# Kernel tuning notes

Measured on AMD Instinct MI355X. Metric: run time of the kernel, lower is better.

The kernel has to match this reference:

```python
import jax, jax.numpy as jnp
import numpy as np

D = 1024
H = 16
EPS = 1e-5


def setup_inputs() -> dict:
    key = jax.random.key(0)
    ks = jax.random.split(key, 6)
    B, T, d = 4, 2048, D
    s = 0.02
    return {
        "x": jax.random.normal(ks[0], (B, T, d), jnp.float32),
        "w_attn": jax.random.normal(ks[1], (d, 3 * d), jnp.float32) * s,
        "w_o": jax.random.normal(ks[2], (d, d), jnp.float32) * s,
        "ln1_g": jnp.ones((d,), jnp.float32),
        "ln1_b": jnp.zeros((d,), jnp.float32),
        "ln2_g": jnp.ones((d,), jnp.float32),
        "ln2_b": jnp.zeros((d,), jnp.float32),
        "w_fc": jax.random.normal(ks[3], (d, 4 * d), jnp.float32) * s,
        "b_fc": jnp.zeros((4 * d,), jnp.float32),
        "w_proj": jax.random.normal(ks[4], (4 * d, d), jnp.float32) * s,
        "b_proj": jnp.zeros((d,), jnp.float32),
    }


def _layernorm(x, g, b):
    mu = jnp.mean(x, axis=-1, keepdims=True)
    var = jnp.mean(jnp.square(x - mu), axis=-1, keepdims=True)
    return (x - mu) * jax.lax.rsqrt(var + EPS) * g + b


def _attention(x, w_attn, w_o):
    B, T, d = x.shape
    hd = d // H
    qkv = x @ w_attn  # [B,T,3d]
    q, k, v = jnp.split(qkv, 3, axis=-1)
    q = q.reshape(B, T, H, hd).transpose(0, 2, 1, 3)  # [B,H,T,hd]
    k = k.reshape(B, T, H, hd).transpose(0, 2, 1, 3)
    v = v.reshape(B, T, H, hd).transpose(0, 2, 1, 3)
    att = jnp.einsum("bhqd,bhkd->bhqk", q, k) * (1.0 / np.sqrt(hd))
    mask = jnp.tril(jnp.ones((T, T), bool))
    att = jnp.where(mask, att, jnp.float32(-jnp.inf))
    att = jax.nn.softmax(att, axis=-1)
    y = jnp.einsum("bhqk,bhkd->bhqd", att, v)
    y = y.transpose(0, 2, 1, 3).reshape(B, T, d)
    return y @ w_o


def reference(x, w_attn, w_o, ln1_g, ln1_b, ln2_g, ln2_b, w_fc, b_fc, w_proj, b_proj):
    x = x + _attention(_layernorm(x, ln1_g, ln1_b), w_attn, w_o)
    h = _layernorm(x, ln2_g, ln2_b)
    h = jax.nn.gelu(h @ w_fc + b_fc, approximate=True)
    return x + h @ w_proj + b_proj
```

## Files before the change

kernel.cpp:

```cpp
#include <hip/hip_runtime.h>
#include <math.h>

#define D_MODEL 1024
#define NHEAD   16
#define HDIM    64
#define SEQ     2048
#define BATCH   4
#define NROWS   (BATCH*SEQ)

using bf16x8 = __attribute__((ext_vector_type(8))) short;
using bf16x4 = __attribute__((ext_vector_type(4))) short;
using f32x4  = __attribute__((ext_vector_type(4))) float;

__device__ __forceinline__ unsigned short f2bf(float f) {
    unsigned u = __float_as_uint(f);
    u += 0x7fffu + ((u >> 16) & 1u);
    return (unsigned short)(u >> 16);
}
__device__ __forceinline__ float bf2f(unsigned short h) {
    unsigned u = ((unsigned)h) << 16;
    return __uint_as_float(u);
}

#define ASYNC_COPY16(g, l) \
    __builtin_amdgcn_global_load_lds((__attribute__((address_space(1))) const void*)(g), \
                                     (__attribute__((address_space(3))) void*)(l), 16, 0, 0)

__global__ __launch_bounds__(256) void ln_kernel(const float* __restrict__ x,
                                                 const float* __restrict__ g,
                                                 const float* __restrict__ b,
                                                 unsigned short* __restrict__ out) {
    const int row = blockIdx.x;
    const int tid = threadIdx.x;
    const float4* x4 = (const float4*)(x + (size_t)row * D_MODEL);
    float4 v = x4[tid];
    float s  = v.x + v.y + v.z + v.w;
    float sq = v.x*v.x + v.y*v.y + v.z*v.z + v.w*v.w;
    #pragma unroll
    for (int off = 32; off >= 1; off >>= 1) {
        s  += __shfl_down(s,  off, 64);
        sq += __shfl_down(sq, off, 64);
    }
    __shared__ float rs[4], rq[4];
    const int wave = tid >> 6;
    if ((tid & 63) == 0) { rs[wave] = s; rq[wave] = sq; }
    __syncthreads();
    const float tot  = rs[0] + rs[1] + rs[2] + rs[3];
    const float totq = rq[0] + rq[1] + rq[2] + rq[3];
    const float mu   = tot * (1.0f / D_MODEL);
    const float var  = totq * (1.0f / D_MODEL) - mu * mu;
    const float rstd = rsqrtf(var + 1e-5f);
    const float4 gv = ((const float4*)g)[tid];
    const float4 bv = ((const float4*)b)[tid];
    unsigned short* o = out + (size_t)row * D_MODEL + tid * 4;
    o[0] = f2bf((v.x - mu) * rstd * gv.x + bv.x);
    o[1] = f2bf((v.y - mu) * rstd * gv.y + bv.y);
    o[2] = f2bf((v.z - mu) * rstd * gv.z + bv.z);
    o[3] = f2bf((v.w - mu) * rstd * gv.w + bv.w);
}

__global__ __launch_bounds__(256) void wt_kernel(const float* __restrict__ w,
                                                 unsigned short* __restrict__ wt,
                                                 int K, int N) {
    __shared__ float tile[32][33];
    const int n0 = blockIdx.x * 32, k0 = blockIdx.y * 32;
    const int tx = threadIdx.x & 31, ty = threadIdx.x >> 5;
    #pragma unroll
    for (int j = 0; j < 4; ++j)
        tile[ty + j * 8][tx] = w[(size_t)(k0 + ty + j * 8) * N + n0 + tx];
    __syncthreads();
    #pragma unroll
    for (int j = 0; j < 4; ++j)
        wt[(size_t)(n0 + ty + j * 8) * K + k0 + tx] = f2bf(tile[tx][ty + j * 8]);
}

template<int MODE>
__global__ __launch_bounds__(256, 2) void gemm_big(const unsigned short* __restrict__ A,
                                                   const unsigned short* __restrict__ Bt,
                                                   const float* __restrict__ bias,
                                                   unsigned short* __restrict__ outp,
                                                   unsigned short* __restrict__ vt_out,
                                                   int M, int N, int K, int Kslice) {
    __shared__ __align__(16) unsigned short As[256 * 64];
    __shared__ __align__(16) unsigned short Bs[128 * 64];

    const int tid  = threadIdx.x;
    const int lane = tid & 63;
    const int wave = __builtin_amdgcn_readfirstlane(tid >> 6);
    const int quad = lane >> 4, l16 = lane & 15;
    const int wm = wave >> 1, wn = wave & 1;
    const int m0 = blockIdx.x * 256, n0 = blockIdx.y * 128;

    int kbeg = 0, klen = K;
    if (MODE == 1) {
        kbeg = blockIdx.z * Kslice;
        klen = (blockIdx.z == gridDim.z - 1) ? (K - kbeg) : Kslice;
    }

    f32x4 acc[8][4] = {};

    const int rr  = tid >> 3;
    const int p   = tid & 7;
    const int gch = (p ^ (rr & 7)) * 8;

    const unsigned short* Ag[8];
    const unsigned short* Bg[4];
    #pragma unroll
    for (int i = 0; i < 8; ++i)
        Ag[i] = A + (size_t)(m0 + i * 32 + rr) * K + gch + kbeg;
    #pragma unroll
    for (int i = 0; i < 4; ++i)
        Bg[i] = Bt + (size_t)(n0 + i * 32 + rr) * K + gch + kbeg;

    const int pc = (quad ^ (l16 & 7)) * 8;

    for (int kb = 0; kb < klen; kb += 64) {
        #pragma unroll
        for (int i = 0; i < 8; ++i)
            ASYNC_COPY16(Ag[i] + kb, As + i * 2048 + tid * 8);
        #pragma unroll
        for (int i = 0; i < 4; ++i)
            ASYNC_COPY16(Bg[i] + kb, Bs + i * 2048 + tid * 8);
        __syncthreads();

        #pragma unroll
        for (int half = 0; half < 2; ++half) {
            const int off = half ? (pc ^ 32) : pc;
            bf16x8 b[4];
            #pragma unroll
            for (int j = 0; j < 4; ++j)
                b[j] = *(const bf16x8*)&Bs[(wn * 64 + j * 16 + l16) * 64 + off];
            #pragma unroll
            for (int i = 0; i < 8; ++i) {
                bf16x8 a = *(const bf16x8*)&As[(wm * 128 + i * 16 + l16) * 64 + off];
                #pragma unroll
                for (int j = 0; j < 4; ++j)
                    acc[i][j] = __builtin_amdgcn_mfma_f32_16x16x32_bf16(a, b[j], acc[i][j], 0, 0, 0);
            }
        }
        __syncthreads();
    }

    if (MODE == 0) {
        #pragma unroll
        for (int i = 0; i < 8; ++i)
          #pragma unroll
          for (int j = 0; j < 4; ++j)
            #pragma unroll
            for (int r = 0; r < 4; ++r) {
                const int row = m0 + wm * 128 + i * 16 + quad * 4 + r;
                const int col = n0 + wn * 64 + j * 16 + l16;
                float v = acc[i][j][r] + bias[col];
                const float u = 0.7978845608028654f * (v + 0.044715f * v * v * v);
                const float e = __expf(2.0f * u);
                v = 0.5f * v * (2.0f - 2.0f / (e + 1.0f));
                outp[(size_t)row * N + col] = f2bf(v);
            }
    } else if (MODE == 1) {
        unsigned short* outb = outp + (size_t)blockIdx.z * M * N;
        #pragma unroll
        for (int i = 0; i < 8; ++i)
          #pragma unroll
          for (int j = 0; j < 4; ++j)
            #pragma unroll
            for (int r = 0; r < 4; ++r) {
                const int row = m0 + wm * 128 + i * 16 + quad * 4 + r;
                const int col = n0 + wn * 64 + j * 16 + l16;
                outb[(size_t)row * N + col] = f2bf(acc[i][j][r]);
            }
    } else {
        if (n0 < 2048) {
            const float sc = (n0 < 1024) ? 0.125f : 1.0f;
            #pragma unroll
            for (int i = 0; i < 8; ++i)
              #pragma unroll
              for (int j = 0; j < 4; ++j)
                #pragma unroll
                for (int r = 0; r < 4; ++r) {
                    const int row = m0 + wm * 128 + i * 16 + quad * 4 + r;
                    const int col = n0 + wn * 64 + j * 16 + l16;
                    outp[(size_t)row * 2048 + col] = f2bf(acc[i][j][r] * sc);
                }
        } else {
            #pragma unroll
            for (int i = 0; i < 8; ++i)
              #pragma unroll
              for (int j = 0; j < 4; ++j) {
                    const int dv  = n0 - 2048 + wn * 64 + j * 16 + l16;
                    const int tok = m0 + wm * 128 + i * 16 + quad * 4;
                    ushort4 pk;
                    pk.x = f2bf(acc[i][j][0]); pk.y = f2bf(acc[i][j][1]);
                    pk.z = f2bf(acc[i][j][2]); pk.w = f2bf(acc[i][j][3]);
                    *(ushort4*)(vt_out + (size_t)dv * NROWS + tok) = pk;
                }
        }
    }
}

template<bool PARTIAL>
__global__ __launch_bounds__(256) void gemm_bt(const unsigned short* __restrict__ A,
                                               const unsigned short* __restrict__ Bt,
                                               unsigned short* __restrict__ outb,
                                               int M, int N, int K, int Kslice) {
    __shared__ __align__(16) unsigned short As[128 * 32];
    __shared__ __align__(16) unsigned short Bs[128 * 32];

    const int tid  = threadIdx.x;
    const int lane = tid & 63;
    const int wave = __builtin_amdgcn_readfirstlane(tid >> 6);
    const int quad = lane >> 4, l16 = lane & 15;
    const int wm = wave >> 1, wn = wave & 1;
    const int m0 = blockIdx.x * 128, n0 = blockIdx.y * 128;
    const int kbeg = PARTIAL ? blockIdx.z * Kslice : 0;
    const int klen = PARTIAL ? ((blockIdx.z == gridDim.z - 1) ? (K - kbeg) : Kslice) : K;

    f32x4 acc[4][4] = {};

    const int rA = tid >> 2;
    const int p  = tid & 3;
    const int cs = (p ^ ((rA >> 1) & 3)) * 8;

    const unsigned short* Ag0 = A  + (size_t)(m0 + rA) * K + cs + kbeg;
    const unsigned short* Ag1 = A  + (size_t)(m0 + rA + 64) * K + cs + kbeg;
    const unsigned short* Bg0 = Bt + (size_t)(n0 + rA) * K + cs + kbeg;
    const unsigned short* Bg1 = Bt + (size_t)(n0 + rA + 64) * K + cs + kbeg;
    unsigned short* Al0 = As + tid * 8;
    unsigned short* Al1 = As + tid * 8 + 2048;
    unsigned short* Bl0 = Bs + tid * 8;
    unsigned short* Bl1 = Bs + tid * 8 + 2048;

    const int sw = (quad ^ ((l16 >> 1) & 3)) * 8;

    for (int kb = 0; kb < klen; kb += 32) {
        ASYNC_COPY16(Ag0 + kb, Al0);
        ASYNC_COPY16(Ag1 + kb, Al1);
        ASYNC_COPY16(Bg0 + kb, Bl0);
        ASYNC_COPY16(Bg1 + kb, Bl1);
        __syncthreads();

        bf16x8 a[4], b[4];
        #pragma unroll
        for (int i = 0; i < 4; ++i)
            a[i] = *(const bf16x8*)&As[(wm * 64 + i * 16 + l16) * 32 + sw];
        #pragma unroll
        for (int j = 0; j < 4; ++j)
            b[j] = *(const bf16x8*)&Bs[(wn * 64 + j * 16 + l16) * 32 + sw];
        #pragma unroll
        for (int i = 0; i < 4; ++i)
            #pragma unroll
            for (int j = 0; j < 4; ++j)
                acc[i][j] = __builtin_amdgcn_mfma_f32_16x16x32_bf16(a[i], b[j], acc[i][j], 0, 0, 0);
        __syncthreads();
    }

    unsigned short* ob = outb;
    if (PARTIAL) ob += (size_t)blockIdx.z * M * N;

    #pragma unroll
    for (int i = 0; i < 4; ++i)
      #pragma unroll
      for (int j = 0; j < 4; ++j)
        #pragma unroll
        for (int r = 0; r < 4; ++r) {
            const int row = m0 + wm * 64 + i * 16 + quad * 4 + r;
            const int col = n0 + wn * 64 + j * 16 + l16;
            ob[(size_t)row * N + col] = f2bf(acc[i][j][r]);
        }
}

__global__ __launch_bounds__(256) void reduce_wo_ln2(const float* __restrict__ x,
                                                     const unsigned short* __restrict__ pw,
                                                     const float* __restrict__ g,
                                                     const float* __restrict__ bb,
                                                     float* __restrict__ out,
                                                     unsigned short* __restrict__ lnout) {
    const int row = blockIdx.x;
    const int tid = threadIdx.x;
    const size_t base = (size_t)row * D_MODEL + tid * 4;
    const size_t stride = (size_t)NROWS * D_MODEL;
    float4 v = *(const float4*)(x + base);
    #pragma unroll
    for (int z = 0; z < 4; ++z) {
        ushort4 a = *(const ushort4*)(pw + z * stride + base);
        v.x += bf2f(a.x); v.y += bf2f(a.y); v.z += bf2f(a.z); v.w += bf2f(a.w);
    }
    *(float4*)(out + base) = v;

    float s  = v.x + v.y + v.z + v.w;
    float sq = v.x*v.x + v.y*v.y + v.z*v.z + v.w*v.w;
    #pragma unroll
    for (int off = 32; off >= 1; off >>= 1) {
        s  += __shfl_down(s,  off, 64);
        sq += __shfl_down(sq, off, 64);
    }
    __shared__ float rs[4], rq[4];
    const int wave = tid >> 6;
    if ((tid & 63) == 0) { rs[wave] = s; rq[wave] = sq; }
    __syncthreads();
    const float tot  = rs[0] + rs[1] + rs[2] + rs[3];
    const float totq = rq[0] + rq[1] + rq[2] + rq[3];
    const float mu   = tot * (1.0f / D_MODEL);
    const float var  = totq * (1.0f / D_MODEL) - mu * mu;
    const float rstd = rsqrtf(var + 1e-5f);
    const float4 gv = ((const float4*)g)[tid];
    const float4 bv = ((const float4*)bb)[tid];
    unsigned short* o = lnout + (size_t)row * D_MODEL + tid * 4;
    o[0] = f2bf((v.x - mu) * rstd * gv.x + bv.x);
    o[1] = f2bf((v.y - mu) * rstd * gv.y + bv.y);
    o[2] = f2bf((v.z - mu) * rstd * gv.z + bv.z);
    o[3] = f2bf((v.w - mu) * rstd * gv.w + bv.w);
}

__global__ __launch_bounds__(256) void reduce_kernel(float* __restrict__ out,
                                                     const unsigned short* __restrict__ pp,
                                                     const float* __restrict__ bias) {
    const int row = blockIdx.x;
    const int c0 = threadIdx.x * 4;
    const size_t base = (size_t)row * D_MODEL + c0;
    const size_t stride = (size_t)NROWS * D_MODEL;
    float4 o = *(float4*)(out + base);
    const float4 bs = *(const float4*)(bias + c0);
    o.x += bs.x; o.y += bs.y; o.z += bs.z; o.w += bs.w;
    #pragma unroll
    for (int z = 0; z < 3; ++z) {
        ushort4 a = *(const ushort4*)(pp + z * stride + base);
        o.x += bf2f(a.x); o.y += bf2f(a.y); o.z += bf2f(a.z); o.w += bf2f(a.w);
    }
    *(float4*)(out + base) = o;
}

__global__ __launch_bounds__(256) void attn_kernel(const unsigned short* __restrict__ qk,
                                                   const unsigned short* __restrict__ VT,
                                                   unsigned short* __restrict__ y) {
    __shared__ __align__(16) unsigned short Qs[128 * 64];
    __shared__ __align__(16) unsigned short Ks[64 * 64];
    __shared__ __align__(16) unsigned short Vs[80 * 64];
    __shared__ __align__(16) unsigned short Ps[128 * 68];

    const int tid  = threadIdx.x;
    const int lane = tid & 63, w = tid >> 6;
    const int quad = lane >> 4, l16 = lane & 15;
    const int s7   = l16 & 7;
    const int pc0  = (quad ^ s7) * 8;
    const int pc1  = ((quad + 4) ^ s7) * 8;
    const int srow = tid >> 3, sp = tid & 7;

    const int pairidx = blockIdx.x;
    const int bh = blockIdx.y;
    const int b = bh >> 4, h = bh & 15;
    const size_t rowbase = (size_t)b * SEQ;
    const unsigned short* Qbase = qk + h * 64;
    const unsigned short* Kbase = qk + 1024 + h * 64;
    const unsigned short* Vbase = VT + (size_t)(h * 64) * NROWS + b * SEQ;

    #pragma unroll
    for (int e = 0; e < 4; ++e) {
        const int off = tid * 4 + e;
        Vs[4096 + off] = (off < 64) ? (unsigned short)0x3F80 : (unsigned short)0;
    }

    for (int phase = 0; phase < 2; ++phase) {
        const int Q = phase ? pairidx : (15 - pairidx);
        const int nkt = 2 * Q + 2;
        const int qg0 = Q * 128;

        #pragma unroll
        for (int i = 0; i < 4; ++i) {
            const int row = i * 32 + srow;
            const int c = sp ^ (row & 7);
            ASYNC_COPY16(Qbase + (rowbase + qg0 + row) * 2048 + c * 8,
                         (char*)Qs + i * 4096 + tid * 16);
        }
        __syncthreads();

        bf16x8 aq[2][2];
        #pragma unroll
        for (int sub = 0; sub < 2; ++sub) {
            const int qrow = sub * 64 + w * 16 + l16;
            aq[sub][0] = *(const bf16x8*)&Qs[qrow * 64 + pc0];
            aq[sub][1] = *(const bf16x8*)&Qs[qrow * 64 + pc1];
        }

        f32x4 o[2][5] = {};

        for (int kt = 0; kt < nkt; ++kt) {
            #pragma unroll
            for (int i = 0; i < 2; ++i) {
                const int row = i * 32 + srow;
                const int c = sp ^ (row & 7);
                ASYNC_COPY16(Kbase + (rowbase + kt * 64 + row) * 2048 + c * 8,
                             (char*)Ks + i * 4096 + tid * 16);
                ASYNC_COPY16(Vbase + (size_t)row * NROWS + kt * 64 + c * 8,
                             (char*)Vs + i * 4096 + tid * 16);
            }
            __syncthreads();

            bf16x8 bk[4][2];
            #pragma unroll
            for (int cb = 0; cb < 4; ++cb) {
                const int krow = cb * 16 + l16;
                bk[cb][0] = *(const bf16x8*)&Ks[krow * 64 + pc0];
                bk[cb][1] = *(const bf16x8*)&Ks[krow * 64 + pc1];
            }

            #pragma unroll
            for (int sub = 0; sub < 2; ++sub) {
                if (kt > 2 * Q + sub) continue;
                f32x4 s[4] = {};
                #pragma unroll
                for (int cb = 0; cb < 4; ++cb) {
                    s[cb] = __builtin_amdgcn_mfma_f32_16x16x32_bf16(aq[sub][0], bk[cb][0], s[cb], 0, 0, 0);
                    s[cb] = __builtin_amdgcn_mfma_f32_16x16x32_bf16(aq[sub][1], bk[cb][1], s[cb], 0, 0, 0);
                }
                const int prow0 = sub * 64 + w * 16 + quad * 4;
                if (kt == 2 * Q + sub) {
                    const int qg = qg0 + prow0;
                    const int kg = kt * 64 + l16;
                    #pragma unroll
                    for (int cb = 0; cb < 4; ++cb)
                        #pragma unroll
                        for (int r = 0; r < 4; ++r) {
                            const float e = __expf(s[cb][r]);
                            const float pv = (kg + cb * 16 > qg + r) ? 0.0f : e;
                            Ps[(prow0 + r) * 68 + cb * 16 + l16] = f2bf(pv);
                        }
                } else {
                    #pragma unroll
                    for (int cb = 0; cb < 4; ++cb)
                        #pragma unroll
                        for (int r = 0; r < 4; ++r)
                            Ps[(prow0 + r) * 68 + cb * 16 + l16] = f2bf(__expf(s[cb][r]));
                }
            }
            __syncthreads();

            bf16x8 bv[5][2];
            #pragma unroll
            for (int db = 0; db < 5; ++db) {
                const int vrow = db * 16 + l16;
                bv[db][0] = *(const bf16x8*)&Vs[vrow * 64 + pc0];
                bv[db][1] = *(const bf16x8*)&Vs[vrow * 64 + pc1];
            }
            #pragma unroll
            for (int sub = 0; sub < 2; ++sub) {
                if (kt > 2 * Q + sub) continue;
                const unsigned short* pb = &Ps[(sub * 64 + w * 16 + l16) * 68];
                bf16x8 ap0, ap1;
                *(bf16x4*)&ap0       = *(const bf16x4*)(pb + quad * 8);
                *((bf16x4*)&ap0 + 1) = *(const bf16x4*)(pb + quad * 8 + 4);
                *(bf16x4*)&ap1       = *(const bf16x4*)(pb + 32 + quad * 8);
                *((bf16x4*)&ap1 + 1) = *(const bf16x4*)(pb + 32 + quad * 8 + 4);
                #pragma unroll
                for (int db = 0; db < 5; ++db) {
                    o[sub][db] = __builtin_amdgcn_mfma_f32_16x16x32_bf16(ap0, bv[db][0], o[sub][db], 0, 0, 0);
                    o[sub][db] = __builtin_amdgcn_mfma_f32_16x16x32_bf16(ap1, bv[db][1], o[sub][db], 0, 0, 0);
                }
            }
            __syncthreads();
        }

        #pragma unroll
        for (int sub = 0; sub < 2; ++sub)
            #pragma unroll
            for (int r = 0; r < 4; ++r) {
                const float lsum = __shfl(o[sub][4][r], lane & 48);
                const float rinv = 1.0f / lsum;
                const int trow = qg0 + sub * 64 + w * 16 + quad * 4 + r;
                unsigned short* yp = y + (rowbase + trow) * (size_t)D_MODEL + h * 64 + l16;
                #pragma unroll
                for (int db = 0; db < 4; ++db)
                    yp[db * 16] = f2bf(o[sub][db][r] * rinv);
            }
    }
}

extern "C" void kernel_launch(void* const* d_in, const int* in_sizes, int n_in,
                              void* d_out, int out_size, void* d_ws, size_t ws_size,
                              hipStream_t stream) {
    (void)in_sizes; (void)n_in; (void)out_size; (void)ws_size;
    const float* x      = (const float*)d_in[0];
    const float* w_attn = (const float*)d_in[1];
    const float* w_o    = (const float*)d_in[2];
    const float* ln1_g  = (const float*)d_in[3];
    const float* ln1_b  = (const float*)d_in[4];
    const float* ln2_g  = (const float*)d_in[5];
    const float* ln2_b  = (const float*)d_in[6];
    const float* w_fc   = (const float*)d_in[7];
    const float* b_fc   = (const float*)d_in[8];
    const float* w_proj = (const float*)d_in[9];
    const float* b_proj = (const float*)d_in[10];
    float* out = (float*)d_out;

    char* ws = (char*)d_ws;
    const size_t MiB = 1048576;
    unsigned short* ln_buf  = (unsigned short*)ws;
    unsigned short* qkbuf   = (unsigned short*)(ws + 16 * MiB);
    unsigned short* VTbuf   = (unsigned short*)(ws + 48 * MiB);
    unsigned short* wt_attn = (unsigned short*)(ws + 64 * MiB);
    unsigned short* hbuf    = (unsigned short*)(ws + 64 * MiB);
    unsigned short* wt_o    = (unsigned short*)(ws + 126 * MiB);
    unsigned short* pw      = (unsigned short*)(ws + 16 * MiB);
    unsigned short* wt_fc   = (unsigned short*)(ws + 48 * MiB);
    unsigned short* wt_proj = (unsigned short*)(ws + 56 * MiB);
    unsigned short* pp      = (unsigned short*)ws;

    wt_kernel<<<dim3(3072 / 32, 1024 / 32), 256, 0, stream>>>(w_attn, wt_attn, 1024, 3072);
    wt_kernel<<<dim3(1024 / 32, 1024 / 32), 256, 0, stream>>>(w_o, wt_o, 1024, 1024);

    ln_kernel<<<NROWS, 256, 0, stream>>>(x, ln1_g, ln1_b, ln_buf);

    gemm_big<2><<<dim3(NROWS / 256, 3072 / 128), 256, 0, stream>>>(
        ln_buf, wt_attn, nullptr, qkbuf, VTbuf, NROWS, 3072, 1024, 0);

    attn_kernel<<<dim3(8, BATCH * NHEAD), 256, 0, stream>>>(qkbuf, VTbuf, ln_buf);

    gemm_bt<true><<<dim3(NROWS / 128, 1024 / 128, 4), 256, 0, stream>>>(
        ln_buf, wt_o, pw, NROWS, 1024, 1024, 256);
    reduce_wo_ln2<<<NROWS, 256, 0, stream>>>(x, pw, ln2_g, ln2_b, out, ln_buf);

    wt_kernel<<<dim3(4096 / 32, 1024 / 32), 256, 0, stream>>>(w_fc, wt_fc, 1024, 4096);
    wt_kernel<<<dim3(1024 / 32, 4096 / 32), 256, 0, stream>>>(w_proj, wt_proj, 4096, 1024);

    gemm_big<0><<<dim3(NROWS / 256, 4096 / 128), 256, 0, stream>>>(
        ln_buf, wt_fc, b_fc, hbuf, nullptr, NROWS, 4096, 1024, 0);

    gemm_big<1><<<dim3(NROWS / 256, 1024 / 128, 3), 256, 0, stream>>>(
        hbuf, wt_proj, nullptr, pp, nullptr, NROWS, 1024, 4096, 1344);
    reduce_kernel<<<NROWS, 256, 0, stream>>>(out, pp, b_proj);
}
```

Measured before the change: 516.4 us.

## Replace GEMMs with 8-wave 256x256 double-buffered LDS pipelined kernel

Introduces gemm8, a 512-thread kernel computing 256x256 output tiles. It double-buffers A and B tiles in 128KB of dynamic shared memory. Async global-to-LDS copies are interleaved with MFMA phases, separated by explicit barriers and s_setprio, so loads overlap compute instead of stalling on each k-step. The kernel is used for all four GEMMs, which also replaces the smaller gemm_bt for the output projection and cuts split-K from 4 and 3 partials to 2. The large LDS footprint likely limits occupancy to one block per CU, and the QKV grid of 384 blocks may leave some CUs idle in the final wave.

After: 515.7 us. About the same (-0.1%).

```diff
diff --git a/kernel.cpp b/kernel.cpp
--- a/kernel.cpp
+++ b/kernel.cpp
@@ -75,71 +75,119 @@
 }
 
 template<int MODE>
-__global__ __launch_bounds__(256, 2) void gemm_big(const unsigned short* __restrict__ A,
-                                                   const unsigned short* __restrict__ Bt,
-                                                   const float* __restrict__ bias,
-                                                   unsigned short* __restrict__ outp,
-                                                   unsigned short* __restrict__ vt_out,
-                                                   int M, int N, int K, int Kslice) {
-    __shared__ __align__(16) unsigned short As[256 * 64];
-    __shared__ __align__(16) unsigned short Bs[128 * 64];
+__global__ __launch_bounds__(512, 2) void gemm8(const unsigned short* __restrict__ A,
+                                                const unsigned short* __restrict__ Bt,
+                                                const float* __restrict__ bias,
+                                                unsigned short* __restrict__ outp,
+                                                unsigned short* __restrict__ vt_out,
+                                                int M, int N, int K, int Kslice) {
+    extern __shared__ __align__(16) char smem[];
 
     const int tid  = threadIdx.x;
     const int lane = tid & 63;
     const int wave = __builtin_amdgcn_readfirstlane(tid >> 6);
     const int quad = lane >> 4, l16 = lane & 15;
-    const int wm = wave >> 1, wn = wave & 1;
-    const int m0 = blockIdx.x * 256, n0 = blockIdx.y * 128;
+    const int wm = wave >> 2, wn = wave & 3;
+    const int m0 = blockIdx.x * 256, n0 = blockIdx.y * 256;
 
     int kbeg = 0, klen = K;
     if (MODE == 1) {
         kbeg = blockIdx.z * Kslice;
-        klen = (blockIdx.z == gridDim.z - 1) ? (K - kbeg) : Kslice;
-    }
+        klen = (blockIdx.z == (int)gridDim.z - 1) ? (K - kbeg) : Kslice;
+    }
+    const int nt = klen >> 6;
+
+    const int r0  = tid >> 2;
+    const int gch = ((tid & 3) ^ (r0 & 3)) * 8;
+    const unsigned short* Ag0 = A  + (size_t)(m0 + r0) * K + gch + kbeg;
+    const unsigned short* Ag1 = Ag0 + (size_t)128 * K;
+    const unsigned short* Bg0 = Bt + (size_t)(n0 + r0) * K + gch + kbeg;
+    const unsigned short* Bg1 = Bg0 + (size_t)128 * K;
+    char* ldsA = smem + tid * 16;
+    char* ldsB = smem + 32768 + tid * 16;
+
+#define STG_A(kh, tt, bb) do { const int ko_ = (tt)*64 + (kh)*32;             \
+        ASYNC_COPY16(Ag0 + ko_, ldsA + (bb)*65536 + (kh)*16384);              \
+        ASYNC_COPY16(Ag1 + ko_, ldsA + (bb)*65536 + (kh)*16384 + 8192); } while (0)
+#define STG_B(kh, tt, bb) do { const int ko_ = (tt)*64 + (kh)*32;             \
+        ASYNC_COPY16(Bg0 + ko_, ldsB + (bb)*65536 + (kh)*16384);              \
+        ASYNC_COPY16(Bg1 + ko_, ldsB + (bb)*65536 + (kh)*16384 + 8192); } while (0)
+
+    const int coff = (quad ^ (l16 & 3)) * 16;
+    const char* rdA = smem + (wm * 128 + l16) * 64 + coff;
+    const char* rdB = smem + 32768 + (wn * 64 + l16) * 64 + coff;
 
     f32x4 acc[8][4] = {};
 
-    const int rr  = tid >> 3;
-    const int p   = tid & 7;
-    const int gch = (p ^ (rr & 7)) * 8;
-
-    const unsigned short* Ag[8];
-    const unsigned short* Bg[4];
-    #pragma unroll
-    for (int i = 0; i < 8; ++i)
-        Ag[i] = A + (size_t)(m0 + i * 32 + rr) * K + gch + kbeg;
-    #pragma unroll
-    for (int i = 0; i < 4; ++i)
-        Bg[i] = Bt + (size_t)(n0 + i * 32 + rr) * K + gch + kbeg;
-
-    const int pc = (quad ^ (l16 & 7)) * 8;
-
-    for (int kb = 0; kb < klen; kb += 64) {
-        #pragma unroll
-        for (int i = 0; i < 8; ++i)
-            ASYNC_COPY16(Ag[i] + kb, As + i * 2048 + tid * 8);
-        #pragma unroll
-        for (int i = 0; i < 4; ++i)
-            ASYNC_COPY16(Bg[i] + kb, Bs + i * 2048 + tid * 8);
-        __syncthreads();
-
-        #pragma unroll
-        for (int half = 0; half < 2; ++half) {
-            const int off = half ? (pc ^ 32) : pc;
-            bf16x8 b[4];
-            #pragma unroll
-            for (int j = 0; j < 4; ++j)
-                b[j] = *(const bf16x8*)&Bs[(wn * 64 + j * 16 + l16) * 64 + off];
-            #pragma unroll
-            for (int i = 0; i < 8; ++i) {
-                bf16x8 a = *(const bf16x8*)&As[(wm * 128 + i * 16 + l16) * 64 + off];
-                #pragma unroll
-                for (int j = 0; j < 4; ++j)
-                    acc[i][j] = __builtin_amdgcn_mfma_f32_16x16x32_bf16(a, b[j], acc[i][j], 0, 0, 0);
-            }
-        }
-        __syncthreads();
-    }
+    STG_A(0, 0, 0); STG_B(0, 0, 0); STG_A(1, 0, 0); STG_B(1, 0, 0);
+    STG_A(0, 1, 1); STG_B(0, 1, 1); STG_A(1, 1, 1);
+    asm volatile("s_waitcnt vmcnt(6)\n\ts_barrier" ::: "memory");
+
+    for (int t = 0; t < nt; ++t) {
+        const int cur = t & 1;
+        const char* bA = rdA + cur * 65536;
+        const char* bB = rdB + cur * 65536;
+        bf16x8 a[8], b0, b1;
+
+        #pragma unroll
+        for (int i = 0; i < 8; ++i) a[i] = *(const bf16x8*)(bA + i * 1024);
+        b0 = *(const bf16x8*)(bB);
+        b1 = *(const bf16x8*)(bB + 1024);
+        if (t + 1 < nt) STG_B(1, t + 1, cur ^ 1);
+        asm volatile("s_barrier" ::: "memory");
+        __builtin_amdgcn_s_setprio(1);
+        #pragma unroll
+        for (int i = 0; i < 8; ++i) {
+            acc[i][0] = __builtin_amdgcn_mfma_f32_16x16x32_bf16(a[i], b0, acc[i][0], 0, 0, 0);
+            acc[i][1] = __builtin_amdgcn_mfma_f32_16x16x32_bf16(a[i], b1, acc[i][1], 0, 0, 0);
+        }
+        __builtin_amdgcn_s_setprio(0);
+        asm volatile("s_barrier" ::: "memory");
+
+        b0 = *(const bf16x8*)(bB + 2048);
+        b1 = *(const bf16x8*)(bB + 3072);
+        if (t + 2 < nt) STG_A(0, t + 2, cur);
+        asm volatile("s_barrier" ::: "memory");
+        __builtin_amdgcn_s_setprio(1);
+        #pragma unroll
+        for (int i = 0; i < 8; ++i) {
+            acc[i][2] = __builtin_amdgcn_mfma_f32_16x16x32_bf16(a[i], b0, acc[i][2], 0, 0, 0);
+            acc[i][3] = __builtin_amdgcn_mfma_f32_16x16x32_bf16(a[i], b1, acc[i][3], 0, 0, 0);
+        }
+        __builtin_amdgcn_s_setprio(0);
+        asm volatile("s_barrier" ::: "memory");
+
+        #pragma unroll
+        for (int i = 0; i < 8; ++i) a[i] = *(const bf16x8*)(bA + 16384 + i * 1024);
+        b0 = *(const bf16x8*)(bB + 16384);
+        b1 = *(const bf16x8*)(bB + 16384 + 1024);
+        if (t + 2 < nt) STG_B(0, t + 2, cur);
+        asm volatile("s_barrier" ::: "memory");
+        __builtin_amdgcn_s_setprio(1);
+        #pragma unroll
+        for (int i = 0; i < 8; ++i) {
+            acc[i][0] = __builtin_amdgcn_mfma_f32_16x16x32_bf16(a[i], b0, acc[i][0], 0, 0, 0);
+            acc[i][1] = __builtin_amdgcn_mfma_f32_16x16x32_bf16(a[i], b1, acc[i][1], 0, 0, 0);
+        }
+        __builtin_amdgcn_s_setprio(0);
+        asm volatile("s_barrier" ::: "memory");
+
+        b0 = *(const bf16x8*)(bB + 16384 + 2048);
+        b1 = *(const bf16x8*)(bB + 16384 + 3072);
+        if (t + 2 < nt) STG_A(1, t + 2, cur);
+        asm volatile("s_barrier" ::: "memory");
+        __builtin_amdgcn_s_setprio(1);
+        #pragma unroll
+        for (int i = 0; i < 8; ++i) {
+            acc[i][2] = __builtin_amdgcn_mfma_f32_16x16x32_bf16(a[i], b0, acc[i][2], 0, 0, 0);
+            acc[i][3] = __builtin_amdgcn_mfma_f32_16x16x32_bf16(a[i], b1, acc[i][3], 0, 0, 0);
+        }
+        __builtin_amdgcn_s_setprio(0);
+        if (t + 2 < nt) asm volatile("s_waitcnt vmcnt(6)\n\ts_barrier" ::: "memory");
+        else            asm volatile("s_waitcnt vmcnt(0)\n\ts_barrier" ::: "memory");
+    }
+#undef STG_A
+#undef STG_B
 
     if (MODE == 0) {
         #pragma unroll
@@ -197,77 +245,7 @@
     }
 }
 
-template<bool PARTIAL>
-__global__ __launch_bounds__(256) void gemm_bt(const unsigned short* __restrict__ A,
-                                               const unsigned short* __restrict__ Bt,
-                                               unsigned short* __restrict__ outb,
-                                               int M, int N, int K, int Kslice) {
-    __shared__ __align__(16) unsigned short As[128 * 32];
-    __shared__ __align__(16) unsigned short Bs[128 * 32];
-
-    const int tid  = threadIdx.x;
-    const int lane = tid & 63;
-    const int wave = __builtin_amdgcn_readfirstlane(tid >> 6);
-    const int quad = lane >> 4, l16 = lane & 15;
-    const int wm = wave >> 1, wn = wave & 1;
-    const int m0 = blockIdx.x * 128, n0 = blockIdx.y * 128;
-    const int kbeg = PARTIAL ? blockIdx.z * Kslice : 0;
-    const int klen = PARTIAL ? ((blockIdx.z == gridDim.z - 1) ? (K - kbeg) : Kslice) : K;
-
-    f32x4 acc[4][4] = {};
-
-    const int rA = tid >> 2;
-    const int p  = tid & 3;
-    const int cs = (p ^ ((rA >> 1) & 3)) * 8;
-
-    const unsigned short* Ag0 = A  + (size_t)(m0 + rA) * K + cs + kbeg;
-    const unsigned short* Ag1 = A  + (size_t)(m0 + rA + 64) * K + cs + kbeg;
-    const unsigned short* Bg0 = Bt + (size_t)(n0 + rA) * K + cs + kbeg;
-    const unsigned short* Bg1 = Bt + (size_t)(n0 + rA + 64) * K + cs + kbeg;
-    unsigned short* Al0 = As + tid * 8;
-    unsigned short* Al1 = As + tid * 8 + 2048;
-    unsigned short* Bl0 = Bs + tid * 8;
-    unsigned short* Bl1 = Bs + tid * 8 + 2048;
-
-    const int sw = (quad ^ ((l16 >> 1) & 3)) * 8;
-
-    for (int kb = 0; kb < klen; kb += 32) {
-        ASYNC_COPY16(Ag0 + kb, Al0);
-        ASYNC_COPY16(Ag1 + kb, Al1);
-        ASYNC_COPY16(Bg0 + kb, Bl0);
-        ASYNC_COPY16(Bg1 + kb, Bl1);
-        __syncthreads();
-
-        bf16x8 a[4], b[4];
-        #pragma unroll
-        for (int i = 0; i < 4; ++i)
-            a[i] = *(const bf16x8*)&As[(wm * 64 + i * 16 + l16) * 32 + sw];
-        #pragma unroll
-        for (int j = 0; j < 4; ++j)
-            b[j] = *(const bf16x8*)&Bs[(wn * 64 + j * 16 + l16) * 32 + sw];
-        #pragma unroll
-        for (int i = 0; i < 4; ++i)
-            #pragma unroll
-            for (int j = 0; j < 4; ++j)
-                acc[i][j] = __builtin_amdgcn_mfma_f32_16x16x32_bf16(a[i], b[j], acc[i][j], 0, 0, 0);
-        __syncthreads();
-    }
-
-    unsigned short* ob = outb;
-    if (PARTIAL) ob += (size_t)blockIdx.z * M * N;
-
-    #pragma unroll
-    for (int i = 0; i < 4; ++i)
-      #pragma unroll
-      for (int j = 0; j < 4; ++j)
-        #pragma unroll
-        for (int r = 0; r < 4; ++r) {
-            const int row = m0 + wm * 64 + i * 16 + quad * 4 + r;
-            const int col = n0 + wn * 64 + j * 16 + l16;
-            ob[(size_t)row * N + col] = f2bf(acc[i][j][r]);
-        }
-}
-
+template<int NP>
 __global__ __launch_bounds__(256) void reduce_wo_ln2(const float* __restrict__ x,
                                                      const unsigned short* __restrict__ pw,
                                                      const float* __restrict__ g,
@@ -280,7 +258,7 @@
     const size_t stride = (size_t)NROWS * D_MODEL;
     float4 v = *(const float4*)(x + base);
     #pragma unroll
-    for (int z = 0; z < 4; ++z) {
+    for (int z = 0; z < NP; ++z) {
         ushort4 a = *(const ushort4*)(pw + z * stride + base);
         v.x += bf2f(a.x); v.y += bf2f(a.y); v.z += bf2f(a.z); v.w += bf2f(a.w);
     }
@@ -311,6 +289,7 @@
     o[3] = f2bf((v.w - mu) * rstd * gv.w + bv.w);
 }
 
+template<int NP>
 __global__ __launch_bounds__(256) void reduce_kernel(float* __restrict__ out,
                                                      const unsigned short* __restrict__ pp,
                                                      const float* __restrict__ bias) {
@@ -322,7 +301,7 @@
     const float4 bs = *(const float4*)(bias + c0);
     o.x += bs.x; o.y += bs.y; o.z += bs.z; o.w += bs.w;
     #pragma unroll
-    for (int z = 0; z < 3; ++z) {
+    for (int z = 0; z < NP; ++z) {
         ushort4 a = *(const ushort4*)(pp + z * stride + base);
         o.x += bf2f(a.x); o.y += bf2f(a.y); o.z += bf2f(a.z); o.w += bf2f(a.w);
     }
@@ -491,6 +470,17 @@
     const float* b_proj = (const float*)d_in[10];
     float* out = (float*)d_out;
 
+    static bool attr_set = false;
+    if (!attr_set) {
+        hipFuncSetAttribute(reinterpret_cast<const void*>(&gemm8<0>),
+                            hipFuncAttributeMaxDynamicSharedMemorySize, 131072);
+        hipFuncSetAttribute(reinterpret_cast<const void*>(&gemm8<1>),
+                            hipFuncAttributeMaxDynamicSharedMemorySize, 131072);
+        hipFuncSetAttribute(reinterpret_cast<const void*>(&gemm8<2>),
+                            hipFuncAttributeMaxDynamicSharedMemorySize, 131072);
+        attr_set = true;
+    }
+
     char* ws = (char*)d_ws;
     const size_t MiB = 1048576;
     unsigned short* ln_buf  = (unsigned short*)ws;
@@ -509,22 +499,22 @@
 
     ln_kernel<<<NROWS, 256, 0, stream>>>(x, ln1_g, ln1_b, ln_buf);
 
-    gemm_big<2><<<dim3(NROWS / 256, 3072 / 128), 256, 0, stream>>>(
+    gemm8<2><<<dim3(NROWS / 256, 3072 / 256), 512, 131072, stream>>>(
         ln_buf, wt_attn, nullptr, qkbuf, VTbuf, NROWS, 3072, 1024, 0);
 
     attn_kernel<<<dim3(8, BATCH * NHEAD), 256, 0, stream>>>(qkbuf, VTbuf, ln_buf);
 
-    gemm_bt<true><<<dim3(NROWS / 128, 1024 / 128, 4), 256, 0, stream>>>(
-        ln_buf, wt_o, pw, NROWS, 1024, 1024, 256);
-    reduce_wo_ln2<<<NROWS, 256, 0, stream>>>(x, pw, ln2_g, ln2_b, out, ln_buf);
+    gemm8<1><<<dim3(NROWS / 256, 1024 / 256, 2), 512, 131072, stream>>>(
+        ln_buf, wt_o, nullptr, pw, nullptr, NROWS, 1024, 1024, 512);
+    reduce_wo_ln2<2><<<NROWS, 256, 0, stream>>>(x, pw, ln2_g, ln2_b, out, ln_buf);
 
     wt_kernel<<<dim3(4096 / 32, 1024 / 32), 256, 0, stream>>>(w_fc, wt_fc, 1024, 4096);
     wt_kernel<<<dim3(1024 / 32, 4096 / 32), 256, 0, stream>>>(w_proj, wt_proj, 4096, 1024);
 
-    gemm_big<0><<<dim3(NROWS / 256, 4096 / 128), 256, 0, stream>>>(
+    gemm8<0><<<dim3(NROWS / 256, 4096 / 256), 512, 131072, stream>>>(
         ln_buf, wt_fc, b_fc, hbuf, nullptr, NROWS, 4096, 1024, 0);
 
-    gemm_big<1><<<dim3(NROWS / 256, 1024 / 128, 3), 256, 0, stream>>>(
-        hbuf, wt_proj, nullptr, pp, nullptr, NROWS, 1024, 4096, 1344);
-    reduce_kernel<<<NROWS, 256, 0, stream>>>(out, pp, b_proj);
-}
+    gemm8<1><<<dim3(NROWS / 256, 1024 / 256, 2), 512, 131072, stream>>>(
+        hbuf, wt_proj, nullptr, pp, nullptr, NROWS, 1024, 4096, 2048);
+    reduce_kernel<2><<<NROWS, 256, 0, stream>>>(out, pp, b_proj);
+}
```
